# Optimization experiments

Hardware: AMD Instinct MI355X
Metric: run time of the kernel (lower is better)

## Reference

```python
import jax, jax.numpy as jnp
import numpy as np

GROUPS = 32
EPS = 1e-5
NUM_HEADS = 8
HEAD_DIM = 64
CHANNELS = 512


def group_norm(x, scale, bias):
    # x: [b, h, w, c]; normalize over (h, w, channels-within-group)
    b, h, w, c = x.shape
    xg = x.reshape(b, h, w, GROUPS, c // GROUPS)
    mean = jnp.mean(xg, axis=(1, 2, 4), keepdims=True)
    var = jnp.var(xg, axis=(1, 2, 4), keepdims=True)
    xg = (xg - mean) * jax.lax.rsqrt(var + EPS)
    return xg.reshape(b, h, w, c) * scale + bias


def setup_inputs() -> dict:
    key = jax.random.key(0)
    ks = jax.random.split(key, 8)
    b, hs, ws, c = 8, 32, 32, CHANNELS
    inner = NUM_HEADS * HEAD_DIM
    return {
        "x": jax.random.normal(ks[0], (b, hs, ws, c), dtype=jnp.float32),
        "t": jax.random.normal(ks[1], (b,), dtype=jnp.float32),
        "gn_scale": jnp.ones((c,), dtype=jnp.float32),
        "gn_bias": jnp.zeros((c,), dtype=jnp.float32),
        "w_qkv": jax.random.normal(ks[2], (c, 3 * inner), dtype=jnp.float32) * 0.02,
        "b_qkv": jnp.zeros((3 * inner,), dtype=jnp.float32),
        "w_out": jax.random.normal(ks[3], (inner, c), dtype=jnp.float32) * 0.02,
        "b_out": jnp.zeros((c,), dtype=jnp.float32),
    }


def reference(x, t, gn_scale, gn_bias, w_qkv, b_qkv, w_out, b_out):
    b, hs, ws, c = x.shape
    # NOTE: original reassigns x = GroupNorm(x); the residual uses the NORMALIZED x.
    xn = group_norm(x, gn_scale, gn_bias)
    x_flat = xn.reshape(b, hs * ws, c)                      # [b, s, c]
    qkv = x_flat @ w_qkv + b_qkv                            # [b, s, 3*nh*hd]
    qkv = qkv.reshape(b, hs * ws, NUM_HEADS, 3 * HEAD_DIM)
    q, k, v = jnp.split(qkv, 3, axis=-1)                    # each [b, s, nh, hd]
    q = q / jnp.sqrt(jnp.float32(HEAD_DIM))
    q = q.transpose(0, 2, 1, 3)                             # [b, nh, s, hd]
    k = k.transpose(0, 2, 1, 3)
    v = v.transpose(0, 2, 1, 3)
    attn = jax.nn.softmax(jnp.einsum('bhqd,bhkd->bhqk', q, k), axis=-1)
    out = jnp.einsum('bhqk,bhkd->bhqd', attn, v)            # [b, nh, s, hd]
    out = out.transpose(0, 2, 1, 3).reshape(b, hs * ws, NUM_HEADS * HEAD_DIM)
    h = out @ w_out + b_out                                 # [b, s, c]
    h = h.reshape(b, hs, ws, c)
    return xn + h
```

## Files before the change

### kernel.cpp

```cpp
#include <hip/hip_runtime.h>
#include <hip/hip_bf16.h>


#define B_    8
#define S_    1024
#define C_    512
#define NH    8
#define HD    64
#define QKVC  1536
#define GROUPS 32
#define GSIZE  16
#define EPSV   1e-5f

using frag8 = __attribute__((ext_vector_type(8))) short;
using f32x4 = __attribute__((ext_vector_type(4))) float;

__device__ __forceinline__ float bf2f(unsigned short u) {
    union { unsigned int i; float f; } v; v.i = ((unsigned int)u) << 16; return v.f;
}
__device__ __forceinline__ unsigned short f2bf(float f) {
    union { float f; unsigned int i; } v; v.f = f;
    unsigned int x = v.i;
    return (unsigned short)((x + 0x7fffu + ((x >> 16) & 1u)) >> 16);
}
__device__ __forceinline__ f32x4 zero4() {
    f32x4 z; z[0] = 0.f; z[1] = 0.f; z[2] = 0.f; z[3] = 0.f; return z;
}
__device__ __forceinline__ void gl_lds(const unsigned short* gp, unsigned short* lp) {
    __builtin_amdgcn_global_load_lds(
        (const __attribute__((address_space(1))) void*)gp,
        (__attribute__((address_space(3))) void*)lp, 16, 0, 0);
}

__global__ __launch_bounds__(256) void transpose_kernel(
        const float* __restrict__ in, unsigned short* __restrict__ out,
        int K, int N) {
    __shared__ float tile[32][33];
    int n0 = blockIdx.x * 32, k0 = blockIdx.y * 32;
    int t = threadIdx.x;
    for (int i = 0; i < 4; ++i) {
        int idx = t + i * 256; int r = idx >> 5, c = idx & 31;
        tile[r][c] = in[(size_t)(k0 + r) * N + n0 + c];
    }
    __syncthreads();
    for (int i = 0; i < 4; ++i) {
        int idx = t + i * 256; int r = idx >> 5, c = idx & 31;
        out[(size_t)(n0 + r) * K + k0 + c] = f2bf(tile[c][r]);
    }
}

__global__ __launch_bounds__(256) void gn_kernel(
        const float* __restrict__ x,
        const float* __restrict__ scale,
        const float* __restrict__ bias,
        unsigned short* __restrict__ xn) {
    int bg = blockIdx.x;
    int b = bg >> 5, g = bg & 31;
    const float* xb = x + (size_t)b * S_ * C_;
    int t = threadIdx.x;

    float sum = 0.f, ss = 0.f;
    for (int i = 0; i < 16; ++i) {
        int idx = t + i * 256;
        int row = idx >> 2, j = idx & 3;
        float4 v = *(const float4*)(xb + (size_t)row * C_ + g * GSIZE + j * 4);
        sum += v.x + v.y + v.z + v.w;
        ss  += v.x * v.x + v.y * v.y + v.z * v.z + v.w * v.w;
    }
    for (int off = 1; off < 64; off <<= 1) {
        sum += __shfl_xor(sum, off);
        ss  += __shfl_xor(ss,  off);
    }
    __shared__ float s_sum[4], s_ss[4];
    int wid = t >> 6;
    if ((t & 63) == 0) { s_sum[wid] = sum; s_ss[wid] = ss; }
    __syncthreads();
    sum = s_sum[0] + s_sum[1] + s_sum[2] + s_sum[3];
    ss  = s_ss[0]  + s_ss[1]  + s_ss[2]  + s_ss[3];
    float mean = sum * (1.f / 16384.f);
    float var  = ss * (1.f / 16384.f) - mean * mean;
    float rinv = rsqrtf(var + EPSV);

    float sc[16], bi[16];
    for (int u = 0; u < 16; ++u) {
        sc[u] = scale[g * GSIZE + u];
        bi[u] = bias[g * GSIZE + u];
    }
    for (int i = 0; i < 16; ++i) {
        int idx = t + i * 256;
        int row = idx >> 2, j = idx & 3;
        float4 v = *(const float4*)(xb + (size_t)row * C_ + g * GSIZE + j * 4);
        int c0 = j * 4;
        float f0 = (v.x - mean) * rinv * sc[c0 + 0] + bi[c0 + 0];
        float f1 = (v.y - mean) * rinv * sc[c0 + 1] + bi[c0 + 1];
        float f2 = (v.z - mean) * rinv * sc[c0 + 2] + bi[c0 + 2];
        float f3 = (v.w - mean) * rinv * sc[c0 + 3] + bi[c0 + 3];
        uint2 o;
        o.x = (unsigned int)f2bf(f0) | ((unsigned int)f2bf(f1) << 16);
        o.y = (unsigned int)f2bf(f2) | ((unsigned int)f2bf(f3) << 16);
        *(uint2*)(xn + (size_t)b * S_ * C_ + (size_t)row * C_ + g * GSIZE + c0) = o;
    }
}

template<int MODE>
__global__ __launch_bounds__(256) void gemm_kernel(
        const unsigned short* __restrict__ A,
        const unsigned short* __restrict__ Bt,
        const float* __restrict__ bias,
        const unsigned short* __restrict__ resid,
        unsigned short* __restrict__ outA,
        unsigned short* __restrict__ outV,
        float* __restrict__ outF,
        int M, int N, int K) {
    __shared__ unsigned short As[128 * 32];
    __shared__ unsigned short Bs[128 * 32];
    int m0 = blockIdx.y * 128, n0 = blockIdx.x * 128;
    int t = threadIdx.x;
    int wid = t >> 6, lane = t & 63;
    int quad = lane >> 4, l16 = lane & 15;
    int wm = (wid >> 1) * 64, wn = (wid & 1) * 64;

    f32x4 acc[4][4];
    for (int mi = 0; mi < 4; ++mi)
        for (int ni = 0; ni < 4; ++ni) acc[mi][ni] = zero4();

    for (int k0 = 0; k0 < K; k0 += 32) {
        __syncthreads();
        for (int i = 0; i < 2; ++i) {
            int idx = i * 256 + t;
            int row = idx >> 2, seg = idx & 3;
            gl_lds(A + (size_t)(m0 + row) * K + k0 + seg * 8,
                   As + (size_t)(i * 256 + wid * 64) * 8);
            gl_lds(Bt + (size_t)(n0 + row) * K + k0 + seg * 8,
                   Bs + (size_t)(i * 256 + wid * 64) * 8);
        }
        __syncthreads();

        frag8 bfrag[4], afrag[4];
        for (int ni = 0; ni < 4; ++ni)
            bfrag[ni] = *(const frag8*)(&Bs[(wn + ni * 16 + l16) * 32 + quad * 8]);
        for (int mi = 0; mi < 4; ++mi)
            afrag[mi] = *(const frag8*)(&As[(wm + mi * 16 + l16) * 32 + quad * 8]);

        for (int mi = 0; mi < 4; ++mi)
            for (int ni = 0; ni < 4; ++ni)
                acc[mi][ni] = __builtin_amdgcn_mfma_f32_16x16x32_bf16(
                    afrag[mi], bfrag[ni], acc[mi][ni], 0, 0, 0);
    }

    for (int ni = 0; ni < 4; ++ni) {
        int c0 = n0 + wn + ni * 16;
        float bv = bias[c0 + l16];
        if (MODE == 0) {
            int h = c0 / 192, rr = c0 % 192;
            if (rr >= 128) {
                int d = rr - 128 + l16;
                int bidx = m0 >> 10;
                unsigned short* vp = outV + (((size_t)bidx * NH + h) * HD + d) * S_
                                   + (m0 & 1023) + wm + quad * 4;
                for (int mi = 0; mi < 4; ++mi) {
                    ushort4 pk;
                    pk.x = f2bf(acc[mi][ni][0] + bv);
                    pk.y = f2bf(acc[mi][ni][1] + bv);
                    pk.z = f2bf(acc[mi][ni][2] + bv);
                    pk.w = f2bf(acc[mi][ni][3] + bv);
                    *(ushort4*)(vp + mi * 16) = pk;
                }
            } else {
                float scl = (rr < 64) ? 0.125f : 1.0f;
                int colk = h * 128 + rr + l16;
                for (int mi = 0; mi < 4; ++mi)
                    for (int r = 0; r < 4; ++r) {
                        int row = m0 + wm + mi * 16 + quad * 4 + r;
                        outA[(size_t)row * 1024 + colk] = f2bf((acc[mi][ni][r] + bv) * scl);
                    }
            }
        } else {
            int col = c0 + l16;
            for (int mi = 0; mi < 4; ++mi)
                for (int r = 0; r < 4; ++r) {
                    int row = m0 + wm + mi * 16 + quad * 4 + r;
                    float v = acc[mi][ni][r] + bv + bf2f(resid[(size_t)row * N + col]);
                    outF[(size_t)row * N + col] = v;
                }
        }
    }
}

__global__ __launch_bounds__(256) void attn_kernel(
        const unsigned short* __restrict__ kq,
        const unsigned short* __restrict__ vT,
        unsigned short* __restrict__ attn_out) {
    int i = blockIdx.x;
    int xcd = i & 7, slot = i >> 3;
    int bh = xcd * 8 + (slot >> 3);
    int qt = slot & 7;
    int b = bh >> 3, h = bh & 7;

    int t = threadIdx.x;
    int wid = t >> 6, lane = t & 63, quad = lane >> 4, l16 = lane & 15;
    int q0 = qt * 128 + wid * 32;

    __shared__ unsigned short Ks[2][2048];
    __shared__ unsigned short Vs[2][2048];
    __shared__ unsigned short Ps[4][32 * 40];

    frag8 qf[2][2];
    for (int mi = 0; mi < 2; ++mi) {
        const unsigned short* qrow = kq + ((size_t)b * S_ + q0 + mi * 16 + l16) * 1024 + h * 128;
        qf[mi][0] = *(const frag8*)(qrow + quad * 8);
        qf[mi][1] = *(const frag8*)(qrow + 32 + quad * 8);
    }
    frag8 ones;
    for (int i2 = 0; i2 < 8; ++i2) ones[i2] = (short)0x3f80;

    f32x4 o[2][4], ol[2];
    for (int mi = 0; mi < 2; ++mi) {
        ol[mi] = zero4();
        for (int dt = 0; dt < 4; ++dt) o[mi][dt] = zero4();
    }

    const unsigned short* kbase = kq + (size_t)b * S_ * 1024 + h * 128 + 64;
    const unsigned short* vbase = vT + ((size_t)b * NH + h) * HD * S_;
    unsigned short* pw = &Ps[wid][0];

    int kdh = wid & 1, krh = wid >> 1;
    int krow = krh * 16 + (lane >> 2);
    int kseg = lane & 3;
    int vd = wid * 16 + (lane >> 2);
    int vseg = lane & 3;

    auto stage = [&](int j0, int buf) {
        gl_lds(kbase + (size_t)(j0 + krow) * 1024 + kdh * 32 + kseg * 8,
               &Ks[buf][kdh * 1024 + krh * 512]);
        gl_lds(vbase + (size_t)vd * S_ + j0 + vseg * 8,
               &Vs[buf][wid * 512]);
    };

    stage(0, 0);

    for (int it = 0; it < S_ / 32; ++it) {
        int cur = it & 1, nxt = cur ^ 1;
        __syncthreads();
        if (it < S_ / 32 - 1) stage((it + 1) * 32, nxt);

        frag8 kf[2][2];
        for (int kh = 0; kh < 2; ++kh)
            for (int dh = 0; dh < 2; ++dh)
                kf[kh][dh] = *(const frag8*)(&Ks[cur][dh * 1024 + (kh * 16 + l16) * 32 + quad * 8]);

        f32x4 s[2][2];
        for (int mi = 0; mi < 2; ++mi)
            for (int kh = 0; kh < 2; ++kh) {
                f32x4 acc = zero4();
                acc = __builtin_amdgcn_mfma_f32_16x16x32_bf16(qf[mi][0], kf[kh][0], acc, 0, 0, 0);
                acc = __builtin_amdgcn_mfma_f32_16x16x32_bf16(qf[mi][1], kf[kh][1], acc, 0, 0, 0);
                s[mi][kh] = acc;
            }

        for (int mi = 0; mi < 2; ++mi)
            for (int kh = 0; kh < 2; ++kh)
                for (int r = 0; r < 4; ++r)
                    pw[(mi * 16 + quad * 4 + r) * 40 + kh * 16 + l16] = f2bf(__expf(s[mi][kh][r]));

        frag8 pf[2];
        pf[0] = *(const frag8*)(&pw[l16 * 40 + quad * 8]);
        pf[1] = *(const frag8*)(&pw[(16 + l16) * 40 + quad * 8]);

        frag8 vf[4];
        for (int dt = 0; dt < 4; ++dt)
            vf[dt] = *(const frag8*)(&Vs[cur][(dt * 16 + l16) * 32 + quad * 8]);

        for (int mi = 0; mi < 2; ++mi) {
            ol[mi] = __builtin_amdgcn_mfma_f32_16x16x32_bf16(pf[mi], ones, ol[mi], 0, 0, 0);
            for (int dt = 0; dt < 4; ++dt)
                o[mi][dt] = __builtin_amdgcn_mfma_f32_16x16x32_bf16(pf[mi], vf[dt], o[mi][dt], 0, 0, 0);
        }
    }

    for (int mi = 0; mi < 2; ++mi)
        for (int r = 0; r < 4; ++r) {
            float inv = 1.0f / ol[mi][r];
            int qrw = q0 + mi * 16 + quad * 4 + r;
            for (int dt = 0; dt < 4; ++dt) {
                int ch = h * HD + dt * 16 + l16;
                attn_out[((size_t)b * S_ + qrw) * C_ + ch] = f2bf(o[mi][dt][r] * inv);
            }
        }
}

extern "C" void kernel_launch(void* const* d_in, const int* in_sizes, int n_in,
                              void* d_out, int out_size, void* d_ws, size_t ws_size,
                              hipStream_t stream) {
    const float* x        = (const float*)d_in[0];
    const float* gn_scale = (const float*)d_in[2];
    const float* gn_bias  = (const float*)d_in[3];
    const float* w_qkv    = (const float*)d_in[4];
    const float* b_qkv    = (const float*)d_in[5];
    const float* w_out    = (const float*)d_in[6];
    const float* b_out    = (const float*)d_in[7];
    float* out = (float*)d_out;

    char* ws = (char*)d_ws;
    unsigned short* xn    = (unsigned short*)(ws);
    unsigned short* kq    = (unsigned short*)(ws + ((size_t)8  << 20));
    unsigned short* attn  = (unsigned short*)(ws + ((size_t)24 << 20));
    unsigned short* vT    = (unsigned short*)(ws + ((size_t)32 << 20));
    unsigned short* wqkvT = (unsigned short*)(ws + ((size_t)40 << 20));
    unsigned short* woutT = (unsigned short*)(ws + ((size_t)40 << 20) + ((size_t)3 << 19));

    transpose_kernel<<<dim3(QKVC / 32, C_ / 32), 256, 0, stream>>>(w_qkv, wqkvT, C_, QKVC);
    transpose_kernel<<<dim3(C_ / 32, C_ / 32), 256, 0, stream>>>(w_out, woutT, C_, C_);

    gn_kernel<<<dim3(B_ * GROUPS), 256, 0, stream>>>(x, gn_scale, gn_bias, xn);

    gemm_kernel<0><<<dim3(QKVC / 128, (B_ * S_) / 128), 256, 0, stream>>>(
        xn, wqkvT, b_qkv, nullptr, kq, vT, nullptr, B_ * S_, QKVC, C_);

    attn_kernel<<<dim3(512), 256, 0, stream>>>(kq, vT, attn);

    gemm_kernel<1><<<dim3(C_ / 128, (B_ * S_) / 128), 256, 0, stream>>>(
        attn, woutT, b_out, xn, nullptr, nullptr, out, B_ * S_, C_, C_);
}
```

Baseline: 178.7 us.

## Double-buffer GEMM LDS staging, use exp2 with folded log2e, pack bf16 stores

Result: faster. 170.7 us (-4.5%).

```diff
diff --git a/kernel.cpp b/kernel.cpp
--- a/kernel.cpp
+++ b/kernel.cpp
@@ -11,6 +11,7 @@
 #define GROUPS 32
 #define GSIZE  16
 #define EPSV   1e-5f
+#define QSCL  0.18033688f
 
 using frag8 = __attribute__((ext_vector_type(8))) short;
 using f32x4 = __attribute__((ext_vector_type(4))) float;
@@ -22,6 +23,17 @@
     union { float f; unsigned int i; } v; v.f = f;
     unsigned int x = v.i;
     return (unsigned short)((x + 0x7fffu + ((x >> 16) & 1u)) >> 16);
+}
+__device__ __forceinline__ unsigned int pk2bf(float a, float b) {
+    union { float f; unsigned int u; } x, y; x.f = a; y.f = b;
+    return __builtin_amdgcn_perm(y.u + 0x8000u, x.u + 0x8000u, 0x07060302u);
+}
+__device__ __forceinline__ float fexp2(float x) {
+#if __has_builtin(__builtin_amdgcn_exp2f)
+    return __builtin_amdgcn_exp2f(x);
+#else
+    return exp2f(x);
+#endif
 }
 __device__ __forceinline__ f32x4 zero4() {
     f32x4 z; z[0] = 0.f; z[1] = 0.f; z[2] = 0.f; z[3] = 0.f; return z;
@@ -112,8 +124,8 @@
         unsigned short* __restrict__ outV,
         float* __restrict__ outF,
         int M, int N, int K) {
-    __shared__ unsigned short As[128 * 32];
-    __shared__ unsigned short Bs[128 * 32];
+    __shared__ unsigned short As[2][128 * 32];
+    __shared__ unsigned short Bs[2][128 * 32];
     int m0 = blockIdx.y * 128, n0 = blockIdx.x * 128;
     int t = threadIdx.x;
     int wid = t >> 6, lane = t & 63;
@@ -124,23 +136,28 @@
     for (int mi = 0; mi < 4; ++mi)
         for (int ni = 0; ni < 4; ++ni) acc[mi][ni] = zero4();
 
-    for (int k0 = 0; k0 < K; k0 += 32) {
+    int srow = t >> 2, sseg = t & 3;
+    auto stage = [&](int k0, int buf) {
+        for (int i = 0; i < 2; ++i) {
+            gl_lds(A + (size_t)(m0 + i * 64 + srow) * K + k0 + sseg * 8,
+                   &As[buf][(size_t)(i * 256 + wid * 64) * 8]);
+            gl_lds(Bt + (size_t)(n0 + i * 64 + srow) * K + k0 + sseg * 8,
+                   &Bs[buf][(size_t)(i * 256 + wid * 64) * 8]);
+        }
+    };
+
+    stage(0, 0);
+    int nk = K >> 5;
+    for (int i = 0; i < nk; ++i) {
         __syncthreads();
-        for (int i = 0; i < 2; ++i) {
-            int idx = i * 256 + t;
-            int row = idx >> 2, seg = idx & 3;
-            gl_lds(A + (size_t)(m0 + row) * K + k0 + seg * 8,
-                   As + (size_t)(i * 256 + wid * 64) * 8);
-            gl_lds(Bt + (size_t)(n0 + row) * K + k0 + seg * 8,
-                   Bs + (size_t)(i * 256 + wid * 64) * 8);
-        }
-        __syncthreads();
+        if (i + 1 < nk) stage((i + 1) << 5, (i + 1) & 1);
+        int buf = i & 1;
 
         frag8 bfrag[4], afrag[4];
         for (int ni = 0; ni < 4; ++ni)
-            bfrag[ni] = *(const frag8*)(&Bs[(wn + ni * 16 + l16) * 32 + quad * 8]);
+            bfrag[ni] = *(const frag8*)(&Bs[buf][(wn + ni * 16 + l16) * 32 + quad * 8]);
         for (int mi = 0; mi < 4; ++mi)
-            afrag[mi] = *(const frag8*)(&As[(wm + mi * 16 + l16) * 32 + quad * 8]);
+            afrag[mi] = *(const frag8*)(&As[buf][(wm + mi * 16 + l16) * 32 + quad * 8]);
 
         for (int mi = 0; mi < 4; ++mi)
             for (int ni = 0; ni < 4; ++ni)
@@ -159,15 +176,13 @@
                 unsigned short* vp = outV + (((size_t)bidx * NH + h) * HD + d) * S_
                                    + (m0 & 1023) + wm + quad * 4;
                 for (int mi = 0; mi < 4; ++mi) {
-                    ushort4 pk;
-                    pk.x = f2bf(acc[mi][ni][0] + bv);
-                    pk.y = f2bf(acc[mi][ni][1] + bv);
-                    pk.z = f2bf(acc[mi][ni][2] + bv);
-                    pk.w = f2bf(acc[mi][ni][3] + bv);
-                    *(ushort4*)(vp + mi * 16) = pk;
+                    uint2 pk;
+                    pk.x = pk2bf(acc[mi][ni][0] + bv, acc[mi][ni][1] + bv);
+                    pk.y = pk2bf(acc[mi][ni][2] + bv, acc[mi][ni][3] + bv);
+                    *(uint2*)(vp + mi * 16) = pk;
                 }
             } else {
-                float scl = (rr < 64) ? 0.125f : 1.0f;
+                float scl = (rr < 64) ? QSCL : 1.0f;
                 int colk = h * 128 + rr + l16;
                 for (int mi = 0; mi < 4; ++mi)
                     for (int r = 0; r < 4; ++r) {
@@ -253,15 +268,22 @@
         for (int mi = 0; mi < 2; ++mi)
             for (int kh = 0; kh < 2; ++kh) {
                 f32x4 acc = zero4();
-                acc = __builtin_amdgcn_mfma_f32_16x16x32_bf16(qf[mi][0], kf[kh][0], acc, 0, 0, 0);
-                acc = __builtin_amdgcn_mfma_f32_16x16x32_bf16(qf[mi][1], kf[kh][1], acc, 0, 0, 0);
+                acc = __builtin_amdgcn_mfma_f32_16x16x32_bf16(kf[kh][0], qf[mi][0], acc, 0, 0, 0);
+                acc = __builtin_amdgcn_mfma_f32_16x16x32_bf16(kf[kh][1], qf[mi][1], acc, 0, 0, 0);
                 s[mi][kh] = acc;
             }
 
         for (int mi = 0; mi < 2; ++mi)
-            for (int kh = 0; kh < 2; ++kh)
-                for (int r = 0; r < 4; ++r)
-                    pw[(mi * 16 + quad * 4 + r) * 40 + kh * 16 + l16] = f2bf(__expf(s[mi][kh][r]));
+            for (int kh = 0; kh < 2; ++kh) {
+                float p0 = fexp2(s[mi][kh][0]);
+                float p1 = fexp2(s[mi][kh][1]);
+                float p2 = fexp2(s[mi][kh][2]);
+                float p3 = fexp2(s[mi][kh][3]);
+                uint2 pk;
+                pk.x = pk2bf(p0, p1);
+                pk.y = pk2bf(p2, p3);
+                *(uint2*)(&pw[(mi * 16 + l16) * 40 + kh * 16 + quad * 4]) = pk;
+            }
 
         frag8 pf[2];
         pf[0] = *(const frag8*)(&pw[l16 * 40 + quad * 8]);
```
